# Performance work log

Measured on AMD Instinct MI355X. Metric: run time of the kernel, lower is better.

## Reference

```python
import jax, jax.numpy as jnp
import numpy as np

B, S, SD, CD, F, H = 64, 2048, 32, 8, 1024, 512
D = CD + 1  # lstm input size


def _uinit(k, shape, fan_in):
    lim = 1.0 / np.sqrt(fan_in)
    return jax.random.uniform(k, shape, minval=-lim, maxval=lim, dtype=jnp.float32)


def setup_inputs() -> dict:
    key = jax.random.key(0)
    ks = jax.random.split(key, 12)
    return {
        "initial_state": jax.random.normal(ks[0], (B, SD), dtype=jnp.float32),
        "rnn_input": jax.random.normal(ks[1], (B, S, D), dtype=jnp.float32),
        # encoder MLP: in->H, H->H, H->F (equinox MLP depth=2, relu hidden, identity final)
        "enc_w0": _uinit(ks[2], (H, SD), SD), "enc_b0": _uinit(ks[3], (H,), SD),
        "enc_w1": _uinit(ks[4], (H, H), H), "enc_b1": _uinit(ks[5], (H,), H),
        "enc_w2": _uinit(ks[6], (F, H), H), "enc_b2": _uinit(ks[7], (F,), H),
        # equinox LSTMCell params: weight_ih (4F,D), weight_hh (4F,F), bias (4F,)
        "w_ih": _uinit(ks[8], (4 * F, D), F), "w_hh": _uinit(ks[9], (4 * F, F), F),
        "bias": _uinit(ks[10], (4 * F,), F),
    }


def reference(initial_state, rnn_input, enc_w0, enc_b0, enc_w1, enc_b1, enc_w2, enc_b2, w_ih, w_hh, bias):
    # encoder MLP -> initial hidden state
    h0 = jax.nn.relu(initial_state @ enc_w0.T + enc_b0)
    h0 = jax.nn.relu(h0 @ enc_w1.T + enc_b1)
    h0 = h0 @ enc_w2.T + enc_b2              # [B, F]
    c0 = jnp.zeros_like(h0)

    xs = jnp.swapaxes(rnn_input, 0, 1)       # [S, B, D]

    def step(carry, x):
        h, c = carry
        lin = x @ w_ih.T + h @ w_hh.T + bias  # [B, 4F]
        i, f, g, o = jnp.split(lin, 4, axis=-1)
        c_new = jax.nn.sigmoid(f) * c + jax.nn.sigmoid(i) * jnp.tanh(g)
        h_new = jax.nn.sigmoid(o) * jnp.tanh(c_new)
        # emit the PRE-step hidden state, matching `(self.cell(input, state), state[0])`
        return (h_new, c_new), h

    (h_last, _), h_seq = jax.lax.scan(step, (h0, c0), xs)
    return h_last, jnp.swapaxes(h_seq, 0, 1)  # [B,F], [B,S,F]
```

## Files before the change

kernel.cpp:

```cpp
#include <hip/hip_runtime.h>
#include <hip/hip_bf16.h>
#include <cstdint>
#include <cstddef>


typedef __bf16 bf16x8_t __attribute__((ext_vector_type(8)));
typedef float f32x4_t __attribute__((ext_vector_type(4)));
typedef int   i32x4_t __attribute__((ext_vector_type(4)));
typedef unsigned long long u64_t;
typedef unsigned long long u64x2_t __attribute__((ext_vector_type(2)));
typedef unsigned short u16x4_t __attribute__((ext_vector_type(4)));

#define WS_TAGS    0
#define WS_HBUF    1048576
#define WS_WSHUF   1310720
#define WS_WAUG    9699328
#define WS_XHAT    9961472
#define WS_H1      18350080
#define WS_H2      18481152

__device__ __forceinline__ unsigned short f2bf(float f) {
  unsigned int u = __float_as_uint(f);
  u = (u + 0x7fffu + ((u >> 16) & 1u)) >> 16;
  return (unsigned short)u;
}
__device__ __forceinline__ float sigm(float x) { return 1.f / (1.f + __expf(-x)); }
__device__ __forceinline__ float tanh_f(float x) {
  float e = __expf(-2.f * fabsf(x));
  float r = (1.f - e) / (1.f + e);
  return copysignf(r, x);
}


__global__ void flumen_enc1(const float* __restrict__ x, const float* __restrict__ W,
                            const float* __restrict__ b, float* __restrict__ h1) {
  const int bb = blockIdx.x;
  const int o  = threadIdx.x;
  const f32x4_t* xr = (const f32x4_t*)(x + bb * 32);
  const f32x4_t* wr = (const f32x4_t*)(W + o * 32);
  float acc = b[o];
#pragma unroll
  for (int q = 0; q < 8; ++q) {
    f32x4_t xv = xr[q], wv = wr[q];
    acc += xv[0] * wv[0] + xv[1] * wv[1] + xv[2] * wv[2] + xv[3] * wv[3];
  }
  h1[bb * 512 + o] = fmaxf(acc, 0.f);
}

__global__ void flumen_enc2(const float* __restrict__ in, const float* __restrict__ W,
                            const float* __restrict__ bv, float* __restrict__ outb) {
  __shared__ float s[64 * 256];
  const int tid = threadIdx.x;
  const int ol = tid & 63, bg = tid >> 6;
  const int o = blockIdx.x * 64 + ol;
  float bias = bv[o];
  float acc[8];
#pragma unroll
  for (int q = 0; q < 8; ++q) acc[q] = bias;
  for (int p = 0; p < 2; ++p) {
    __syncthreads();
    for (int i = tid; i < 4096; i += 512) {
      int flat = i * 4;
      int bb = flat >> 8, kk = flat & 255;
      *(f32x4_t*)(s + flat) = *(const f32x4_t*)(in + bb * 512 + p * 256 + kk);
    }
    __syncthreads();
    for (int kk = 0; kk < 256; kk += 4) {
      f32x4_t wv = *(const f32x4_t*)(W + o * 512 + p * 256 + kk);
#pragma unroll
      for (int j = 0; j < 4; ++j) {
        float wj = wv[j];
#pragma unroll
        for (int q = 0; q < 8; ++q)
          acc[q] += wj * s[(bg * 8 + q) * 256 + kk + j];
      }
    }
  }
#pragma unroll
  for (int q = 0; q < 8; ++q)
    outb[(bg * 8 + q) * 512 + o] = fmaxf(acc[q], 0.f);
}

__global__ void flumen_enc3(const float* __restrict__ in, const float* __restrict__ W,
                            const float* __restrict__ bv, float* __restrict__ dout,
                            unsigned short* __restrict__ hbuf) {
  __shared__ float s[64 * 256];
  const int tid = threadIdx.x;
  const int ol = tid & 63, bg = tid >> 6;
  const int o = blockIdx.x * 64 + ol;
  float bias = bv[o];
  float acc[8];
#pragma unroll
  for (int q = 0; q < 8; ++q) acc[q] = bias;
  for (int p = 0; p < 2; ++p) {
    __syncthreads();
    for (int i = tid; i < 4096; i += 512) {
      int flat = i * 4;
      int bb = flat >> 8, kk = flat & 255;
      *(f32x4_t*)(s + flat) = *(const f32x4_t*)(in + bb * 512 + p * 256 + kk);
    }
    __syncthreads();
    for (int kk = 0; kk < 256; kk += 4) {
      f32x4_t wv = *(const f32x4_t*)(W + o * 512 + p * 256 + kk);
#pragma unroll
      for (int j = 0; j < 4; ++j) {
        float wj = wv[j];
#pragma unroll
        for (int q = 0; q < 8; ++q)
          acc[q] += wj * s[(bg * 8 + q) * 256 + kk + j];
      }
    }
  }
  float* out_hseq = dout + 65536;
#pragma unroll
  for (int q = 0; q < 8; ++q) {
    int bb = bg * 8 + q;
    float v = acc[q];
    out_hseq[(size_t)bb * 2097152 + o] = v;
    hbuf[(o >> 5) * 2048 + bb * 32 + (o & 31)] = f2bf(v);
  }
}


__global__ void flumen_wshuf(const float* __restrict__ src, unsigned short* __restrict__ dst) {
  int idx = blockIdx.x * 512 + threadIdx.x;
  int lane = idx & 63, kt = (idx >> 6) & 31, mt = idx >> 11;
  int r = lane & 15;
  int g = r & 3, f = mt * 4 + (r >> 2);
  int k0 = kt * 32 + (lane >> 4) * 8;
  const float* sp = src + (size_t)(g * 1024 + f) * 1024 + k0;
  f32x4_t v0 = *(const f32x4_t*)(sp);
  f32x4_t v1 = *(const f32x4_t*)(sp + 4);
  u16x4_t o0, o1;
#pragma unroll
  for (int j = 0; j < 4; ++j) { o0[j] = f2bf(v0[j]); o1[j] = f2bf(v1[j]); }
  u16x4_t* dp = (u16x4_t*)(dst + (size_t)idx * 8);
  dp[0] = o0; dp[1] = o1;
}

__global__ void flumen_waugi(const float* __restrict__ wih, const float* __restrict__ bias,
                             unsigned short* __restrict__ dst) {
  int idx = blockIdx.x * 512 + threadIdx.x;
  int lane = idx & 63, mt = idx >> 6;
  int r = lane & 15;
  int g = r & 3, f = mt * 4 + (r >> 2);
  int k0 = (lane >> 4) * 8;
  unsigned short o[8];
#pragma unroll
  for (int j = 0; j < 8; ++j) {
    int k = k0 + j;
    float v = (k < 9) ? wih[(size_t)(g * 1024 + f) * 9 + k]
                      : (k == 9 ? bias[g * 1024 + f] : 0.f);
    o[j] = f2bf(v);
  }
  u16x4_t* dp = (u16x4_t*)(dst + (size_t)idx * 8);
  dp[0] = *(u16x4_t*)&o[0];
  dp[1] = *(u16x4_t*)&o[4];
}

__global__ void flumen_convx(const float* __restrict__ xin, unsigned short* __restrict__ dst) {
  int i = (blockIdx.x * 512 + threadIdx.x) * 4;
  int b = i >> 16, t = (i >> 5) & 2047, c0 = i & 31;
  u16x4_t o;
#pragma unroll
  for (int j = 0; j < 4; ++j) {
    int cc = c0 + j;
    float v = (cc < 9) ? xin[((size_t)b * 2048 + t) * 9 + cc] : (cc == 9 ? 1.f : 0.f);
    o[j] = f2bf(v);
  }
  *(u16x4_t*)(dst + ((size_t)t * 64 + b) * 32 + c0) = o;
}

__global__ __launch_bounds__(512, 1) void flumen_lstm(
    const unsigned short* __restrict__ Wshuf,
    const unsigned short* __restrict__ WaugI,
    const unsigned short* __restrict__ Xhat,
    unsigned short* hbuf, int* tags, float* out)
{
  __shared__ __align__(16) char smem[140544];
  char*  h_lds = smem;
  float* hs    = (float*)(smem + 131072);

  float* out_hlast = out;
  float* out_hseq  = out + 65536;
  const int w    = blockIdx.x;
  const int tid  = threadIdx.x;
  const int lane = tid & 63;
  const int m    = tid >> 6;
  const int l15  = lane & 15;
  const int l4   = lane >> 4;
  const int s    = l15 & 7;
  const int Bbase0 = l15 * 2048 + ((l4 ^ (s & 3)) << 4) + ((s >> 2) << 6);

  bf16x8_t Apin[32];
  {
    const char* ap = (const char*)Wshuf + ((size_t)(w * 8 + m) * 32) * 1024 + lane * 16;
#pragma unroll
    for (int kt = 0; kt < 32; ++kt)
      Apin[kt] = *(const bf16x8_t*)(ap + kt * 1024);
  }
  const bf16x8_t wfragI =
      *(const bf16x8_t*)((const char*)WaugI + (size_t)(w * 8 + m) * 1024 + lane * 16);

  int lds_addr[16];
#pragma unroll
  for (int i = 0; i < 16; ++i) {
    int goff = i * 8192 + tid * 16;
    int b = (goff >> 6) & 63;
    int o16 = ((goff >> 12) << 2) | ((goff >> 4) & 3);
    lds_addr[i] = b * 2048 + ((o16 ^ (b & 7)) << 4);
  }

  float carr[4] = {0.f, 0.f, 0.f, 0.f};

  for (int t = 0; t < 2048; ++t) {
    bf16x8_t xf[4];
#pragma unroll
    for (int n = 0; n < 4; ++n)
      xf[n] = *(const bf16x8_t*)(Xhat + ((size_t)t * 64 + n * 16 + l15) * 32 + l4 * 8);

    if (t > 0) {
      if (lane < 32) {
        const char* tp = (const char*)tags + ((size_t)(t - 1) * 32 + lane) * 16;
        int iter = 0;
        while (true) {
          i32x4_t tv;
          asm volatile("global_load_dwordx4 %0, %1, off sc1\n\ts_waitcnt vmcnt(0)"
                       : "=v"(tv) : "v"(tp) : "memory");
          bool good = (tv[0] == t) && (tv[1] == t) && (tv[2] == t) && (tv[3] == t);
          if (__all(good) || ++iter >= (1 << 20)) break;
        }
      }
      __builtin_amdgcn_sched_barrier(0);
    }

    {
      const char* src0 = (const char*)hbuf + (size_t)((t & 1) * 131072) + tid * 16;
      f32x4_t v[8];
#pragma unroll
      for (int i = 0; i < 8; ++i)
        asm volatile("global_load_dwordx4 %0, %1, off sc1"
                     : "=v"(v[i]) : "v"(src0 + i * 8192) : "memory");
      asm volatile("s_waitcnt vmcnt(0)" ::: "memory");
      __builtin_amdgcn_sched_barrier(0);
#pragma unroll
      for (int i = 0; i < 8; ++i)
        *(f32x4_t*)(h_lds + lds_addr[i]) = v[i];
#pragma unroll
      for (int i = 0; i < 8; ++i)
        asm volatile("global_load_dwordx4 %0, %1, off sc1"
                     : "=v"(v[i]) : "v"(src0 + (i + 8) * 8192) : "memory");
      asm volatile("s_waitcnt vmcnt(0)" ::: "memory");
      __builtin_amdgcn_sched_barrier(0);
#pragma unroll
      for (int i = 0; i < 8; ++i)
        *(f32x4_t*)(h_lds + lds_addr[i + 8]) = v[i];
    }
    __syncthreads();

#pragma unroll
    for (int n = 0; n < 4; ++n) {
      f32x4_t acc = __builtin_amdgcn_mfma_f32_16x16x32_bf16(
          wfragI, xf[n], (f32x4_t){0.f, 0.f, 0.f, 0.f}, 0, 0, 0);
      const int bb = Bbase0 + n * 32768;
#pragma unroll
      for (int kt = 0; kt < 32; ++kt) {
        bf16x8_t bf = *(const bf16x8_t*)(h_lds + (bb ^ (kt << 6)));
        acc = __builtin_amdgcn_mfma_f32_16x16x32_bf16(Apin[kt], bf, acc, 0, 0, 0);
      }
      float c = sigm(acc[1]) * carr[n] + sigm(acc[0]) * tanh_f(acc[2]);
      carr[n] = c;
      float h = sigm(acc[3]) * tanh_f(c);
      if (t < 2047) {
        hs[(n * 16 + l15) * 36 + m * 4 + l4] = h;
      } else {
        out_hlast[(n * 16 + l15) * 1024 + w * 32 + m * 4 + l4] = h;
      }
    }

    if (t < 2047) {
      __syncthreads();
      if (m < 4) {
        int b = m * 16 + (lane >> 2), fq = lane & 3;
        f32x4_t u0 = *(const f32x4_t*)(hs + b * 36 + fq * 8);
        f32x4_t u1 = *(const f32x4_t*)(hs + b * 36 + fq * 8 + 4);
        u64_t lo = (u64_t)f2bf(u0[0]) | ((u64_t)f2bf(u0[1]) << 16)
                 | ((u64_t)f2bf(u0[2]) << 32) | ((u64_t)f2bf(u0[3]) << 48);
        u64_t hi = (u64_t)f2bf(u1[0]) | ((u64_t)f2bf(u1[1]) << 16)
                 | ((u64_t)f2bf(u1[2]) << 32) | ((u64_t)f2bf(u1[3]) << 48);
        u64x2_t q = {lo, hi};
        char* dst = (char*)hbuf + (size_t)(((t + 1) & 1) * 131072)
                  + w * 4096 + b * 64 + fq * 16;
        asm volatile("global_store_dwordx4 %0, %1, off sc1" :: "v"(dst), "v"(q) : "memory");
        asm volatile("s_waitcnt vmcnt(0)" ::: "memory");
        if (lane == 0) {
          int* tp = tags + ((size_t)t * 32 + w) * 4 + m;
          int val = t + 1;
          asm volatile("global_store_dword %0, %1, off sc1" :: "v"(tp), "v"(val) : "memory");
        }
      } else {
        int b = (m - 4) * 16 + (lane >> 2), sg = lane & 3;
        float* hd = out_hseq + ((size_t)b * 2048 + (size_t)(t + 1)) * 1024 + w * 32 + sg * 8;
        *(f32x4_t*)hd       = *(const f32x4_t*)(hs + b * 36 + sg * 8);
        *(f32x4_t*)(hd + 4) = *(const f32x4_t*)(hs + b * 36 + sg * 8 + 4);
      }
    }
  }
}


extern "C" void kernel_launch(void* const* d_in, const int* in_sizes, int n_in,
                              void* d_out, int out_size, void* d_ws, size_t ws_size,
                              hipStream_t stream) {
  const float* initial_state = (const float*)d_in[0];
  const float* rnn_input     = (const float*)d_in[1];
  const float* enc_w0        = (const float*)d_in[2];
  const float* enc_b0        = (const float*)d_in[3];
  const float* enc_w1        = (const float*)d_in[4];
  const float* enc_b1        = (const float*)d_in[5];
  const float* enc_w2        = (const float*)d_in[6];
  const float* enc_b2        = (const float*)d_in[7];
  const float* w_ih          = (const float*)d_in[8];
  const float* w_hh          = (const float*)d_in[9];
  const float* bias          = (const float*)d_in[10];

  char* ws = (char*)d_ws;
  int*            tags  = (int*)(ws + WS_TAGS);
  unsigned short* hbuf  = (unsigned short*)(ws + WS_HBUF);
  unsigned short* Wshuf = (unsigned short*)(ws + WS_WSHUF);
  unsigned short* WaugI = (unsigned short*)(ws + WS_WAUG);
  unsigned short* Xhat  = (unsigned short*)(ws + WS_XHAT);
  float*          h1    = (float*)(ws + WS_H1);
  float*          h2    = (float*)(ws + WS_H2);
  float*          out   = (float*)d_out;

  hipMemsetAsync(tags, 0, 1048576, stream);
  flumen_enc1<<<64, 512, 0, stream>>>(initial_state, enc_w0, enc_b0, h1);
  flumen_enc2<<<8, 512, 0, stream>>>(h1, enc_w1, enc_b1, h2);
  flumen_enc3<<<16, 512, 0, stream>>>(h2, enc_w2, enc_b2, out, hbuf);
  flumen_wshuf<<<1024, 512, 0, stream>>>(w_hh, Wshuf);
  flumen_waugi<<<32, 512, 0, stream>>>(w_ih, bias, WaugI);
  flumen_convx<<<2048, 512, 0, stream>>>(rnn_input, Xhat);
  flumen_lstm<<<32, 512, 0, stream>>>(Wshuf, WaugI, Xhat, hbuf, tags, out);
}
```

Measured before the change: 19.28 ms.

## Specialize waves into compute and store roles with MFMA-fragment hbuf layout

Result: slower. 48.95 ms (+153.9%).

```diff
diff --git a/kernel.cpp b/kernel.cpp
--- a/kernel.cpp
+++ b/kernel.cpp
@@ -117,7 +117,9 @@
     int bb = bg * 8 + q;
     float v = acc[q];
     out_hseq[(size_t)bb * 2097152 + o] = v;
-    hbuf[(o >> 5) * 2048 + bb * 32 + (o & 31)] = f2bf(v);
+    int blk  = (bb >> 4) * 32 + (o >> 5);
+    int lane = ((o >> 3) & 3) * 16 + (bb & 15);
+    hbuf[blk * 512 + lane * 8 + (o & 7)] = f2bf(v);
   }
 }
 
@@ -177,7 +179,7 @@
     const unsigned short* __restrict__ Xhat,
     unsigned short* hbuf, int* tags, float* out)
 {
-  __shared__ __align__(16) char smem[140544];
+  __shared__ __align__(16) char smem[140288];
   char*  h_lds = smem;
   float* hs    = (float*)(smem + 131072);
 
@@ -186,38 +188,40 @@
   const int w    = blockIdx.x;
   const int tid  = threadIdx.x;
   const int lane = tid & 63;
-  const int m    = tid >> 6;
+  const int wave = tid >> 6;
   const int l15  = lane & 15;
   const int l4   = lane >> 4;
-  const int s    = l15 & 7;
-  const int Bbase0 = l15 * 2048 + ((l4 ^ (s & 3)) << 4) + ((s >> 2) << 6);
-
-  bf16x8_t Apin[32];
-  {
-    const char* ap = (const char*)Wshuf + ((size_t)(w * 8 + m) * 32) * 1024 + lane * 16;
-#pragma unroll
-    for (int kt = 0; kt < 32; ++kt)
-      Apin[kt] = *(const bf16x8_t*)(ap + kt * 1024);
-  }
-  const bf16x8_t wfragI =
-      *(const bf16x8_t*)((const char*)WaugI + (size_t)(w * 8 + m) * 1024 + lane * 16);
-
-  int lds_addr[16];
-#pragma unroll
-  for (int i = 0; i < 16; ++i) {
-    int goff = i * 8192 + tid * 16;
-    int b = (goff >> 6) & 63;
-    int o16 = ((goff >> 12) << 2) | ((goff >> 4) & 3);
-    lds_addr[i] = b * 2048 + ((o16 ^ (b & 7)) << 4);
-  }
-
-  float carr[4] = {0.f, 0.f, 0.f, 0.f};
+  const bool is_compute = (wave < 4);
+  const int cw = wave & 3;
+
+  bf16x8_t Apin[2][32];
+  bf16x8_t wfragI[2];
+  if (is_compute) {
+#pragma unroll
+    for (int q = 0; q < 2; ++q) {
+      const size_t mt = (size_t)(w * 8 + cw * 2 + q);
+      const char* ap = (const char*)Wshuf + mt * 32768 + lane * 16;
+#pragma unroll
+      for (int kt = 0; kt < 32; ++kt)
+        Apin[q][kt] = *(const bf16x8_t*)(ap + kt * 1024);
+      wfragI[q] = *(const bf16x8_t*)((const char*)WaugI + mt * 1024 + lane * 16);
+    }
+  }
+
+  float carr[2][4] = {{0.f,0.f,0.f,0.f},{0.f,0.f,0.f,0.f}};
 
   for (int t = 0; t < 2048; ++t) {
-    bf16x8_t xf[4];
-#pragma unroll
-    for (int n = 0; n < 4; ++n)
-      xf[n] = *(const bf16x8_t*)(Xhat + ((size_t)t * 64 + n * 16 + l15) * 32 + l4 * 8);
+    f32x4_t acc[2][4];
+    if (is_compute) {
+#pragma unroll
+      for (int n = 0; n < 4; ++n) {
+        bf16x8_t xf = *(const bf16x8_t*)(Xhat + ((size_t)t * 64 + n * 16 + l15) * 32 + l4 * 8);
+#pragma unroll
+        for (int q = 0; q < 2; ++q)
+          acc[q][n] = __builtin_amdgcn_mfma_f32_16x16x32_bf16(
+              wfragI[q], xf, (f32x4_t){0.f, 0.f, 0.f, 0.f}, 0, 0, 0);
+      }
+    }
 
     if (t > 0) {
       if (lane < 32) {
@@ -245,7 +249,7 @@
       __builtin_amdgcn_sched_barrier(0);
 #pragma unroll
       for (int i = 0; i < 8; ++i)
-        *(f32x4_t*)(h_lds + lds_addr[i]) = v[i];
+        *(f32x4_t*)(h_lds + tid * 16 + i * 8192) = v[i];
 #pragma unroll
       for (int i = 0; i < 8; ++i)
         asm volatile("global_load_dwordx4 %0, %1, off sc1"
@@ -254,56 +258,59 @@
       __builtin_amdgcn_sched_barrier(0);
 #pragma unroll
       for (int i = 0; i < 8; ++i)
-        *(f32x4_t*)(h_lds + lds_addr[i + 8]) = v[i];
-    }
-    __syncthreads();
-
-#pragma unroll
-    for (int n = 0; n < 4; ++n) {
-      f32x4_t acc = __builtin_amdgcn_mfma_f32_16x16x32_bf16(
-          wfragI, xf[n], (f32x4_t){0.f, 0.f, 0.f, 0.f}, 0, 0, 0);
-      const int bb = Bbase0 + n * 32768;
-#pragma unroll
-      for (int kt = 0; kt < 32; ++kt) {
-        bf16x8_t bf = *(const bf16x8_t*)(h_lds + (bb ^ (kt << 6)));
-        acc = __builtin_amdgcn_mfma_f32_16x16x32_bf16(Apin[kt], bf, acc, 0, 0, 0);
-      }
-      float c = sigm(acc[1]) * carr[n] + sigm(acc[0]) * tanh_f(acc[2]);
-      carr[n] = c;
-      float h = sigm(acc[3]) * tanh_f(c);
-      if (t < 2047) {
-        hs[(n * 16 + l15) * 36 + m * 4 + l4] = h;
-      } else {
-        out_hlast[(n * 16 + l15) * 1024 + w * 32 + m * 4 + l4] = h;
-      }
-    }
-
-    if (t < 2047) {
-      __syncthreads();
-      if (m < 4) {
-        int b = m * 16 + (lane >> 2), fq = lane & 3;
-        f32x4_t u0 = *(const f32x4_t*)(hs + b * 36 + fq * 8);
-        f32x4_t u1 = *(const f32x4_t*)(hs + b * 36 + fq * 8 + 4);
-        u64_t lo = (u64_t)f2bf(u0[0]) | ((u64_t)f2bf(u0[1]) << 16)
-                 | ((u64_t)f2bf(u0[2]) << 32) | ((u64_t)f2bf(u0[3]) << 48);
-        u64_t hi = (u64_t)f2bf(u1[0]) | ((u64_t)f2bf(u1[1]) << 16)
-                 | ((u64_t)f2bf(u1[2]) << 32) | ((u64_t)f2bf(u1[3]) << 48);
-        u64x2_t q = {lo, hi};
-        char* dst = (char*)hbuf + (size_t)(((t + 1) & 1) * 131072)
-                  + w * 4096 + b * 64 + fq * 16;
-        asm volatile("global_store_dwordx4 %0, %1, off sc1" :: "v"(dst), "v"(q) : "memory");
-        asm volatile("s_waitcnt vmcnt(0)" ::: "memory");
-        if (lane == 0) {
-          int* tp = tags + ((size_t)t * 32 + w) * 4 + m;
-          int val = t + 1;
-          asm volatile("global_store_dword %0, %1, off sc1" :: "v"(tp), "v"(val) : "memory");
+        *(f32x4_t*)(h_lds + tid * 16 + (i + 8) * 8192) = v[i];
+    }
+    __syncthreads();
+
+    if (is_compute) {
+#pragma unroll
+      for (int n = 0; n < 4; ++n) {
+        const char* bb = h_lds + n * 32768 + lane * 16;
+#pragma unroll
+        for (int kt = 0; kt < 32; ++kt) {
+          bf16x8_t bf = *(const bf16x8_t*)(bb + kt * 1024);
+          acc[0][n] = __builtin_amdgcn_mfma_f32_16x16x32_bf16(Apin[0][kt], bf, acc[0][n], 0, 0, 0);
+          acc[1][n] = __builtin_amdgcn_mfma_f32_16x16x32_bf16(Apin[1][kt], bf, acc[1][n], 0, 0, 0);
         }
-      } else {
-        int b = (m - 4) * 16 + (lane >> 2), sg = lane & 3;
-        float* hd = out_hseq + ((size_t)b * 2048 + (size_t)(t + 1)) * 1024 + w * 32 + sg * 8;
-        *(f32x4_t*)hd       = *(const f32x4_t*)(hs + b * 36 + sg * 8);
-        *(f32x4_t*)(hd + 4) = *(const f32x4_t*)(hs + b * 36 + sg * 8 + 4);
-      }
+      }
+#pragma unroll
+      for (int q = 0; q < 2; ++q)
+#pragma unroll
+        for (int n = 0; n < 4; ++n) {
+          float c = sigm(acc[q][n][1]) * carr[q][n] + sigm(acc[q][n][0]) * tanh_f(acc[q][n][2]);
+          carr[q][n] = c;
+          float h = sigm(acc[q][n][3]) * tanh_f(c);
+          if (t < 2047) {
+            hs[(n * 16 + l15) * 36 + (cw * 2 + q) * 4 + l4] = h;
+          } else {
+            out_hlast[(n * 16 + l15) * 1024 + w * 32 + (cw * 2 + q) * 4 + l4] = h;
+          }
+        }
+    }
+    __syncthreads();
+
+    if (!is_compute && t < 2047) {
+      const int b = cw * 16 + l15;
+      f32x4_t u0 = *(const f32x4_t*)(hs + b * 36 + l4 * 8);
+      f32x4_t u1 = *(const f32x4_t*)(hs + b * 36 + l4 * 8 + 4);
+      u64_t lo = (u64_t)f2bf(u0[0]) | ((u64_t)f2bf(u0[1]) << 16)
+               | ((u64_t)f2bf(u0[2]) << 32) | ((u64_t)f2bf(u0[3]) << 48);
+      u64_t hi = (u64_t)f2bf(u1[0]) | ((u64_t)f2bf(u1[1]) << 16)
+               | ((u64_t)f2bf(u1[2]) << 32) | ((u64_t)f2bf(u1[3]) << 48);
+      u64x2_t q = {lo, hi};
+      char* dst = (char*)hbuf + (size_t)(((t + 1) & 1) * 131072)
+                + (cw * 32 + w) * 1024 + lane * 16;
+      asm volatile("global_store_dwordx4 %0, %1, off sc1" :: "v"(dst), "v"(q) : "memory");
+      asm volatile("s_waitcnt vmcnt(0)" ::: "memory");
+      if (lane == 0) {
+        int* tp = tags + ((size_t)t * 32 + w) * 4 + cw;
+        int val = t + 1;
+        asm volatile("global_store_dword %0, %1, off sc1" :: "v"(tp), "v"(val) : "memory");
+      }
+      int b2 = cw * 16 + (lane >> 2), sg = lane & 3;
+      float* hd = out_hseq + ((size_t)b2 * 2048 + (size_t)(t + 1)) * 1024 + w * 32 + sg * 8;
+      *(f32x4_t*)hd       = *(const f32x4_t*)(hs + b2 * 36 + sg * 8);
+      *(f32x4_t*)(hd + 4) = *(const f32x4_t*)(hs + b2 * 36 + sg * 8 + 4);
     }
   }
 }
```
